# Performance work log

Hardware: AMD Instinct MI355X
Metric: run time of the kernel (lower is better)

Reference implementation:

```python
import jax, jax.numpy as jnp
import numpy as np

GAMMA = 0.99  # init kwarg


def _discounted_returns(ep_rs):
    # reversed running_add = running_add*gamma + r, emitted per step
    def step(carry, r):
        carry = carry * GAMMA + r
        return carry, carry
    _, out = jax.lax.scan(step, jnp.float32(0.0), ep_rs, reverse=True)
    return out  # [T]


def setup_inputs() -> dict:
    key = jax.random.key(0)
    k1, k2, k3 = jax.random.split(key, 3)
    T, A = 2097152, 18
    weight = jax.random.normal(k1, (T, A), dtype=jnp.float32)
    ep_rs = jax.random.normal(k2, (T,), dtype=jnp.float32)
    ep_as = jax.random.randint(k3, (T,), 0, A, dtype=jnp.int64)
    return {"weight": weight, "ep_rs": ep_rs, "ep_as": ep_as}


def reference(weight, ep_rs, ep_as):
    d = _discounted_returns(ep_rs)
    d = d - jnp.mean(d)
    # cross_entropy with reduction='none': -log_softmax(weight)[t, ep_as[t]]
    logp = jax.nn.log_softmax(weight, axis=-1)  # [T, A]
    neg_log_prob = -jnp.take_along_axis(logp, ep_as[:, None], axis=-1)[:, 0]  # [T]
    return jnp.mean(neg_log_prob * d)
```

## Files before the change

### kernel.cpp

```cpp
#include <hip/hip_runtime.h>
#include <math.h>

#define T_TOTAL 2097152
#define A_DIM   18
#define GAMMA_D 0.99

#define CHUNK 256
#define NC    (T_TOTAL / CHUNK)
#define KTR   14

__device__ inline void pow_tid(double base, int e, double& out) {
    double p = 1.0, b = base;
    #pragma unroll
    for (int bit = 0; bit < 8; ++bit) {
        if (e & (1 << bit)) p *= b;
        b *= b;
    }
    out = p;
}

__global__ void k_local(const float* __restrict__ r, double* __restrict__ L) {
    const int tid  = blockIdx.x * blockDim.x + threadIdx.x;
    const int c    = tid >> 6;
    const int lane = tid & 63;
    const float4 v = ((const float4*)r)[(size_t)c * 64 + lane];
    const double g = GAMMA_D;
    double p;
    pow_tid(g, 4 * lane, p);
    double w = p * ((double)v.x + g * ((double)v.y + g * ((double)v.z + g * (double)v.w)));
    #pragma unroll
    for (int off = 32; off > 0; off >>= 1) w += __shfl_down(w, off, 64);
    if (lane == 0) L[c] = w;
}

__global__ void k_carry(const double* __restrict__ L, double* __restrict__ carry,
                        double G) {
    const int c = blockIdx.x * blockDim.x + threadIdx.x;
    double acc = 0.0, w = 1.0;
    #pragma unroll
    for (int m = 0; m < KTR; ++m) {
        int idx = c + 1 + m;
        if (idx < NC) acc += w * L[idx];
        w *= G;
    }
    carry[c] = acc;
}

__launch_bounds__(256)
__global__ void k_main(const float* __restrict__ wgt, const int* __restrict__ act,
                       const float* __restrict__ r, const double* __restrict__ carry,
                       double* __restrict__ partials) {
    __shared__ float  lds[CHUNK * A_DIM];
    __shared__ double ldsT[4];
    __shared__ double red[12];
    const int tid  = threadIdx.x;
    const int lane = tid & 63, wv = tid >> 6;
    const int c    = blockIdx.x;
    const double g = GAMMA_D;
    double p, ip;
    pow_tid(g, tid, p);
    pow_tid(1.0 / g, tid, ip);
    const double g256 = 0.076314983205510425;

    const float4* src = (const float4*)(wgt + (size_t)c * CHUNK * A_DIM);
    float4* dst = (float4*)lds;
    #pragma unroll
    for (int i = 0; i < 5; ++i) {
        int idx = tid + 256 * i;
        if (idx < CHUNK * A_DIM / 4) dst[idx] = src[idx];
    }
    const int row = c * CHUNK + tid;
    double ss = p * (double)r[row];
    #pragma unroll
    for (int off = 1; off < 64; off <<= 1) {
        double v = __shfl_down(ss, off, 64);
        ss += (lane + off < 64) ? v : 0.0;
    }
    if (lane == 0) ldsT[wv] = ss;
    __syncthreads();
    double tail = 0.0;
    #pragma unroll
    for (int m = 0; m < 4; ++m)
        if (m > wv) tail += ldsT[m];
    const double dval = ip * (ss + tail + g256 * carry[c]);

    const float* wr = lds + tid * A_DIM;
    float mx = wr[0];
    #pragma unroll
    for (int j = 1; j < A_DIM; ++j) mx = fmaxf(mx, wr[j]);
    float s = 0.0f;
    #pragma unroll
    for (int j = 0; j < A_DIM; ++j) s += expf(wr[j] - mx);
    const float nlp = mx + logf(s) - wr[act[row]];

    double s_d  = dval;
    double s_n  = (double)nlp;
    double s_nd = (double)nlp * dval;

    #pragma unroll
    for (int off = 32; off > 0; off >>= 1) {
        s_d  += __shfl_down(s_d,  off, 64);
        s_n  += __shfl_down(s_n,  off, 64);
        s_nd += __shfl_down(s_nd, off, 64);
    }
    if (lane == 0) { red[wv*3+0] = s_d; red[wv*3+1] = s_n; red[wv*3+2] = s_nd; }
    __syncthreads();
    if (tid == 0) {
        double a = 0.0, b = 0.0, cc = 0.0;
        #pragma unroll
        for (int i = 0; i < 4; ++i) { a += red[i*3]; b += red[i*3+1]; cc += red[i*3+2]; }
        partials[c*3+0] = a;
        partials[c*3+1] = b;
        partials[c*3+2] = cc;
    }
}

__global__ void k_final(const double* __restrict__ partials, float* __restrict__ out) {
    __shared__ double red[12];
    const int tid = threadIdx.x;
    double a = 0.0, b = 0.0, c = 0.0;
    for (int i = tid; i < NC; i += 256) {
        a += partials[i*3+0];
        b += partials[i*3+1];
        c += partials[i*3+2];
    }
    #pragma unroll
    for (int off = 32; off > 0; off >>= 1) {
        a += __shfl_down(a, off, 64);
        b += __shfl_down(b, off, 64);
        c += __shfl_down(c, off, 64);
    }
    const int lane = tid & 63, wv = tid >> 6;
    if (lane == 0) { red[wv*3+0] = a; red[wv*3+1] = b; red[wv*3+2] = c; }
    __syncthreads();
    if (tid == 0) {
        double A_ = 0.0, B_ = 0.0, C_ = 0.0;
        #pragma unroll
        for (int i = 0; i < 4; ++i) { A_ += red[i*3]; B_ += red[i*3+1]; C_ += red[i*3+2]; }
        const double invT = 1.0 / (double)T_TOTAL;
        out[0] = (float)((C_ - (A_ * invT) * B_) * invT);
    }
}

extern "C" void kernel_launch(void* const* d_in, const int* in_sizes, int n_in,
                              void* d_out, int out_size, void* d_ws, size_t ws_size,
                              hipStream_t stream) {
    const float* weight = (const float*)d_in[0];
    const float* ep_rs  = (const float*)d_in[1];
    const int*   ep_as  = (const int*)  d_in[2];
    float* out = (float*)d_out;

    char* ws = (char*)d_ws;
    double* L        = (double*)(ws);
    double* carry    = (double*)(ws + (1 << 16));
    double* partials = (double*)(ws + (2 << 16));

    const double G = pow(GAMMA_D, (double)CHUNK);

    k_local <<<T_TOTAL / 4 / 256, 256, 0, stream>>>(ep_rs, L);
    k_carry <<<NC / 256,          256, 0, stream>>>(L, carry, G);
    k_main  <<<NC,                256, 0, stream>>>(weight, ep_as, ep_rs, carry, partials);
    k_final <<<1,                 256, 0, stream>>>(partials, out);
}
```

Measured before the change: 241.5 us.

## Defer chunk carry into final reduction, drop separate local-sum and carry kernels

Removes the k_local and k_carry kernels. The main kernel now writes each chunk's local discounted sum plus extra partials (sum of nlp*gamma^-t). Because the carry term enters the per-row value linearly, the final kernel rebuilds each chunk's carry with a truncated backward recurrence and folds it in algebraically. This saves two launches and an extra pass over the rewards. In exchange, the single-block final kernel does serial per-thread loops over 32 chunks each, and each chunk now writes 5 partials instead of 3.

Measured after the change: 243.6 us. About the same (+0.8%).

```diff
diff --git a/kernel.cpp b/kernel.cpp
--- a/kernel.cpp
+++ b/kernel.cpp
@@ -8,59 +8,30 @@
 #define CHUNK 256
 #define NC    (T_TOTAL / CHUNK)
 #define KTR   14
+#define G256  0.076314983205510425
 
-__device__ inline void pow_tid(double base, int e, double& out) {
+__device__ inline double pow_tid(double base, int e) {
     double p = 1.0, b = base;
     #pragma unroll
     for (int bit = 0; bit < 8; ++bit) {
         if (e & (1 << bit)) p *= b;
         b *= b;
     }
-    out = p;
-}
-
-__global__ void k_local(const float* __restrict__ r, double* __restrict__ L) {
-    const int tid  = blockIdx.x * blockDim.x + threadIdx.x;
-    const int c    = tid >> 6;
-    const int lane = tid & 63;
-    const float4 v = ((const float4*)r)[(size_t)c * 64 + lane];
-    const double g = GAMMA_D;
-    double p;
-    pow_tid(g, 4 * lane, p);
-    double w = p * ((double)v.x + g * ((double)v.y + g * ((double)v.z + g * (double)v.w)));
-    #pragma unroll
-    for (int off = 32; off > 0; off >>= 1) w += __shfl_down(w, off, 64);
-    if (lane == 0) L[c] = w;
-}
-
-__global__ void k_carry(const double* __restrict__ L, double* __restrict__ carry,
-                        double G) {
-    const int c = blockIdx.x * blockDim.x + threadIdx.x;
-    double acc = 0.0, w = 1.0;
-    #pragma unroll
-    for (int m = 0; m < KTR; ++m) {
-        int idx = c + 1 + m;
-        if (idx < NC) acc += w * L[idx];
-        w *= G;
-    }
-    carry[c] = acc;
+    return p;
 }
 
 __launch_bounds__(256)
 __global__ void k_main(const float* __restrict__ wgt, const int* __restrict__ act,
-                       const float* __restrict__ r, const double* __restrict__ carry,
-                       double* __restrict__ partials) {
+                       const float* __restrict__ r, double* __restrict__ partials) {
     __shared__ float  lds[CHUNK * A_DIM];
     __shared__ double ldsT[4];
-    __shared__ double red[12];
+    __shared__ double red[16];
     const int tid  = threadIdx.x;
     const int lane = tid & 63, wv = tid >> 6;
     const int c    = blockIdx.x;
-    const double g = GAMMA_D;
-    double p, ip;
-    pow_tid(g, tid, p);
-    pow_tid(1.0 / g, tid, ip);
-    const double g256 = 0.076314983205510425;
+    const double g  = GAMMA_D;
+    const double p  = pow_tid(g, tid);
+    const double ip = pow_tid(1.0 / g, tid);
 
     const float4* src = (const float4*)(wgt + (size_t)c * CHUNK * A_DIM);
     float4* dst = (float4*)lds;
@@ -82,7 +53,8 @@
     #pragma unroll
     for (int m = 0; m < 4; ++m)
         if (m > wv) tail += ldsT[m];
-    const double dval = ip * (ss + tail + g256 * carry[c]);
+    const double Lc = ss + tail;
+    const double dl = ip * Lc;
 
     const float* wr = lds + tid * A_DIM;
     float mx = wr[0];
@@ -93,45 +65,71 @@
     for (int j = 0; j < A_DIM; ++j) s += expf(wr[j] - mx);
     const float nlp = mx + logf(s) - wr[act[row]];
 
-    double s_d  = dval;
-    double s_n  = (double)nlp;
-    double s_nd = (double)nlp * dval;
+    double s_dl  = dl;
+    double s_n   = (double)nlp;
+    double s_ndl = (double)nlp * dl;
+    double s_p   = (double)nlp * ip;
 
     #pragma unroll
     for (int off = 32; off > 0; off >>= 1) {
-        s_d  += __shfl_down(s_d,  off, 64);
-        s_n  += __shfl_down(s_n,  off, 64);
-        s_nd += __shfl_down(s_nd, off, 64);
+        s_dl  += __shfl_down(s_dl,  off, 64);
+        s_n   += __shfl_down(s_n,   off, 64);
+        s_ndl += __shfl_down(s_ndl, off, 64);
+        s_p   += __shfl_down(s_p,   off, 64);
     }
-    if (lane == 0) { red[wv*3+0] = s_d; red[wv*3+1] = s_n; red[wv*3+2] = s_nd; }
+    if (lane == 0) {
+        red[wv*4+0] = s_dl; red[wv*4+1] = s_n;
+        red[wv*4+2] = s_ndl; red[wv*4+3] = s_p;
+    }
     __syncthreads();
     if (tid == 0) {
-        double a = 0.0, b = 0.0, cc = 0.0;
+        double a = 0.0, b = 0.0, cc = 0.0, d = 0.0;
         #pragma unroll
-        for (int i = 0; i < 4; ++i) { a += red[i*3]; b += red[i*3+1]; cc += red[i*3+2]; }
-        partials[c*3+0] = a;
-        partials[c*3+1] = b;
-        partials[c*3+2] = cc;
+        for (int i = 0; i < 4; ++i) {
+            a += red[i*4+0]; b += red[i*4+1]; cc += red[i*4+2]; d += red[i*4+3];
+        }
+        double* out5 = partials + (size_t)c * 5;
+        out5[0] = Lc;
+        out5[1] = a;
+        out5[2] = b;
+        out5[3] = cc;
+        out5[4] = d;
     }
 }
 
 __global__ void k_final(const double* __restrict__ partials, float* __restrict__ out) {
     __shared__ double red[12];
     const int tid = threadIdx.x;
-    double a = 0.0, b = 0.0, c = 0.0;
-    for (int i = tid; i < NC; i += 256) {
-        a += partials[i*3+0];
-        b += partials[i*3+1];
-        c += partials[i*3+2];
+    const double g = GAMMA_D, G = G256;
+    const int lo = tid * (NC / 256), hi = lo + (NC / 256) - 1;
+
+    double carry = 0.0, w = 1.0;
+    #pragma unroll
+    for (int m = 0; m < KTR; ++m) {
+        int idx = hi + 1 + m;
+        if (idx < NC) carry += w * partials[(size_t)idx * 5 + 0];
+        w *= G;
     }
+    const double K0 = (1.0 / G - 1.0) / (1.0 / g - 1.0);
+
+    double a = 0.0, b = 0.0, cc = 0.0;
+    for (int c = hi; c >= lo; --c) {
+        if (c != hi) carry = partials[(size_t)(c + 1) * 5 + 0] + G * carry;
+        const double* p5 = partials + (size_t)c * 5;
+        const double gc = G * carry;
+        a  += p5[1] + gc * K0;
+        b  += p5[2];
+        cc += p5[3] + gc * p5[4];
+    }
+
     #pragma unroll
     for (int off = 32; off > 0; off >>= 1) {
-        a += __shfl_down(a, off, 64);
-        b += __shfl_down(b, off, 64);
-        c += __shfl_down(c, off, 64);
+        a  += __shfl_down(a,  off, 64);
+        b  += __shfl_down(b,  off, 64);
+        cc += __shfl_down(cc, off, 64);
     }
     const int lane = tid & 63, wv = tid >> 6;
-    if (lane == 0) { red[wv*3+0] = a; red[wv*3+1] = b; red[wv*3+2] = c; }
+    if (lane == 0) { red[wv*3+0] = a; red[wv*3+1] = b; red[wv*3+2] = cc; }
     __syncthreads();
     if (tid == 0) {
         double A_ = 0.0, B_ = 0.0, C_ = 0.0;
@@ -150,15 +148,8 @@
     const int*   ep_as  = (const int*)  d_in[2];
     float* out = (float*)d_out;
 
-    char* ws = (char*)d_ws;
-    double* L        = (double*)(ws);
-    double* carry    = (double*)(ws + (1 << 16));
-    double* partials = (double*)(ws + (2 << 16));
+    double* partials = (double*)d_ws;
 
-    const double G = pow(GAMMA_D, (double)CHUNK);
-
-    k_local <<<T_TOTAL / 4 / 256, 256, 0, stream>>>(ep_rs, L);
-    k_carry <<<NC / 256,          256, 0, stream>>>(L, carry, G);
-    k_main  <<<NC,                256, 0, stream>>>(weight, ep_as, ep_rs, carry, partials);
-    k_final <<<1,                 256, 0, stream>>>(partials, out);
+    k_main  <<<NC, 256, 0, stream>>>(weight, ep_as, ep_rs, partials);
+    k_final <<<1,  256, 0, stream>>>(partials, out);
 }
```
